# Kernel optimization log

Hardware: AMD Instinct MI355X
Metric: run time of the kernel (lower is better)

Reference implementation:

```python
import jax, jax.numpy as jnp
import numpy as np

D_MODEL = 1024
N_HEADS = 16
DH = (D_MODEL // N_HEADS) // 2  # depth // 2 = 32
B, S = 4, 2048


def setup_inputs() -> dict:
    key = jax.random.key(0)
    ks = jax.random.split(key, 8)
    scale_in = 1.0
    q = jax.random.normal(ks[0], (B, S, D_MODEL), dtype=jnp.float32)
    k = jax.random.normal(ks[1], (B, S, D_MODEL), dtype=jnp.float32)
    v = jax.random.normal(ks[2], (B, S, D_MODEL), dtype=jnp.float32)
    # Per-head projection weights stacked over the head axis (glorot-ish init)
    w_std = (2.0 / (D_MODEL + DH)) ** 0.5
    Wq = jax.random.normal(ks[3], (N_HEADS, D_MODEL, DH), dtype=jnp.float32) * w_std
    Wk = jax.random.normal(ks[4], (N_HEADS, D_MODEL, DH), dtype=jnp.float32) * w_std
    Wv = jax.random.normal(ks[5], (N_HEADS, D_MODEL, DH), dtype=jnp.float32) * w_std
    wo_std = (2.0 / (N_HEADS * DH + D_MODEL)) ** 0.5
    Wo = jax.random.normal(ks[6], (N_HEADS * DH, D_MODEL), dtype=jnp.float32) * wo_std
    return {"q": q, "k": k, "v": v, "Wq": Wq, "Wk": Wk, "Wv": Wv, "Wo": Wo}


def reference(q, k, v, Wq, Wk, Wv, Wo):
    # NOTE: source scales by d_model**-0.5 (not head_dim**-0.5)
    scale = D_MODEL ** (-0.5)
    Q = jnp.einsum("bsd,hde->bhse", q, Wq)   # [B,H,S,DH]
    K = jnp.einsum("btd,hde->bhte", k, Wk)
    V = jnp.einsum("btd,hde->bhte", v, Wv)
    attn = jnp.einsum("bhse,bhte->bhst", Q, K) * scale  # [B,H,S,S]
    attn = jax.nn.softmax(attn, axis=-1)
    x = jnp.einsum("bhst,bhte->bhse", attn, V)  # [B,H,S,DH]
    # concat heads along feature dim (head order = concat order in source)
    x = jnp.transpose(x, (0, 2, 1, 3)).reshape(q.shape[0], q.shape[1], N_HEADS * DH)
    return x @ Wo  # [B,S,D_MODEL]; dropout is identity (training=False)
```

## Files before the change

### kernel.cpp

```cpp
#include <hip/hip_runtime.h>
#include <hip/hip_bf16.h>

typedef __attribute__((ext_vector_type(8))) short short8;
typedef __attribute__((ext_vector_type(4))) float f32x4;
typedef __attribute__((ext_vector_type(4))) float fv4;
typedef __attribute__((ext_vector_type(4))) unsigned int u32x4;

#define MFMA16(a, b, c) __builtin_amdgcn_mfma_f32_16x16x32_bf16((a), (b), (c), 0, 0, 0)

typedef const __attribute__((address_space(1))) unsigned int gu32;
typedef __attribute__((address_space(3))) unsigned int lu32;

__device__ __forceinline__ short f2b(float f) {
  unsigned int x = __builtin_bit_cast(unsigned int, f);
  x += 0x7fffu + ((x >> 16) & 1u);
  return (short)(x >> 16);
}

__device__ __forceinline__ unsigned int cvtpk(float lo, float hi) {
  unsigned int r;
  asm("v_cvt_pk_bf16_f32 %0, %1, %2" : "=v"(r) : "v"(lo), "v"(hi));
  return r;
}

#define hexp2(x) __builtin_amdgcn_exp2f(x)

__global__ void prep_weights(const float* __restrict__ Wq, const float* __restrict__ Wk,
                             const float* __restrict__ Wv, const float* __restrict__ Wo,
                             short* __restrict__ WqT, short* __restrict__ WkT,
                             short* __restrict__ WvT, short* __restrict__ WoT) {
  const float SC2 = 0.045084220027780106f;
  int idx = blockIdx.x * 256 + threadIdx.x;
  if (idx < 3 * 512 * 1024) {
    int wsel = idx >> 19;
    int rem = idx & ((1 << 19) - 1);
    int n = rem >> 10;
    int d = rem & 1023;
    const float* W = (wsel == 0) ? Wq : ((wsel == 1) ? Wk : Wv);
    short* WT = (wsel == 0) ? WqT : ((wsel == 1) ? WkT : WvT);
    float v = W[(n >> 5) * (1024 * 32) + d * 32 + (n & 31)];
    if (wsel == 0) v *= SC2;
    WT[n * 1024 + d] = f2b(v);
  } else {
    int idx2 = idx - 3 * 512 * 1024;
    int n = idx2 >> 9;
    int kk = idx2 & 511;
    WoT[n * 512 + kk] = f2b(Wo[kk * 1024 + n]);
  }
}

__global__ __launch_bounds__(256, 3) void proj_gemm(
    const float* __restrict__ q, const float* __restrict__ k, const float* __restrict__ v,
    const short* __restrict__ WqT, const short* __restrict__ WkT, const short* __restrict__ WvT,
    short* __restrict__ Qb, short* __restrict__ Kb, short* __restrict__ Vtb) {
  __shared__ char smem[49152];
  const int tid = threadIdx.x;
  const int lane = tid & 63;
  const int w = tid >> 6;
  const int l15 = lane & 15, g = lane >> 4;
  const int wm = (w >> 1) * 64, wn = (w & 1) * 64;
  const int id = blockIdx.x;
  const int bm = id & 63;
  const int r = id >> 6;
  const int bn = r & 3;
  const int z = r >> 2;
  const float* A = (z == 0) ? q : ((z == 1) ? k : v);
  const short* BT = (z == 0) ? WqT : ((z == 1) ? WkT : WvT);
  const int bm0 = bm * 128, bn0 = bn * 128;

  const int arow = lane >> 4;
  const int au = lane & 15;
  const int brow = lane >> 3;
  const int bu = lane & 7;

  f32x4 zf = {0.f, 0.f, 0.f, 0.f};
  f32x4 acc[4][4];
#pragma unroll
  for (int a = 0; a < 4; ++a)
#pragma unroll
    for (int bq = 0; bq < 4; ++bq) acc[a][bq] = zf;

  for (int k0 = 0; k0 < 1024; k0 += 64) {
#pragma unroll
    for (int i = 0; i < 8; ++i) {
      int row = 32 * w + 4 * i + arow;
      int u = au ^ (row & 7);
      __builtin_amdgcn_global_load_lds(
          (gu32*)(A + (size_t)(bm0 + row) * 1024 + k0 + 4 * u),
          (lu32*)(smem + w * 8192 + i * 1024), 16, 0, 0);
    }
#pragma unroll
    for (int i = 0; i < 4; ++i) {
      int row = 32 * w + 8 * i + brow;
      int u = bu ^ (row & 7);
      __builtin_amdgcn_global_load_lds(
          (gu32*)(BT + (size_t)(bn0 + row) * 1024 + k0 + 8 * u),
          (lu32*)(smem + 32768 + w * 4096 + i * 1024), 16, 0, 0);
    }
    __syncthreads();

#pragma unroll
    for (int kk = 0; kk < 2; ++kk) {
      short8 af[4], bfr[4];
#pragma unroll
      for (int mf = 0; mf < 4; ++mf) {
        int row = wm + mf * 16 + l15;
        int u0 = 8 * kk + 2 * g;
        fv4 a0 = *(const fv4*)(smem + row * 256 + ((u0 ^ (row & 7)) * 16));
        fv4 a1 = *(const fv4*)(smem + row * 256 + (((u0 + 1) ^ (row & 7)) * 16));
        u32x4 wv;
        wv[0] = cvtpk(a0[0], a0[1]);
        wv[1] = cvtpk(a0[2], a0[3]);
        wv[2] = cvtpk(a1[0], a1[1]);
        wv[3] = cvtpk(a1[2], a1[3]);
        af[mf] = __builtin_bit_cast(short8, wv);
      }
#pragma unroll
      for (int nf = 0; nf < 4; ++nf) {
        int row = wn + nf * 16 + l15;
        int c = 4 * kk + g;
        bfr[nf] = *(const short8*)(smem + 32768 + row * 128 + ((c ^ (row & 7)) * 16));
      }
#pragma unroll
      for (int mf = 0; mf < 4; ++mf)
#pragma unroll
        for (int nf = 0; nf < 4; ++nf)
          acc[mf][nf] = MFMA16(af[mf], bfr[nf], acc[mf][nf]);
    }
    __syncthreads();
  }

#pragma unroll
  for (int mf = 0; mf < 4; ++mf)
#pragma unroll
    for (int nf = 0; nf < 4; ++nf)
#pragma unroll
      for (int i = 0; i < 4; ++i) {
        int row = bm0 + wm + mf * 16 + g * 4 + i;
        int col = bn0 + wn + nf * 16 + l15;
        int bb = row >> 11, ss = row & 2047;
        int hh = col >> 5, ee = col & 31;
        short val = f2b(acc[mf][nf][i]);
        if (z == 2)
          Vtb[((size_t)(bb * 16 + hh) * 32 + ee) * 2048 + ss] = val;
        else if (z == 1)
          Kb[((size_t)(bb * 16 + hh) * 2048 + ss) * 32 + ee] = val;
        else
          Qb[((size_t)(bb * 16 + hh) * 2048 + ss) * 32 + ee] = val;
      }
}

__global__ __launch_bounds__(256, 2) void out_gemm(const short* __restrict__ X,
                                                   const short* __restrict__ WoT,
                                                   float* __restrict__ out) {
  __shared__ char smem[32768];
  const int tid = threadIdx.x;
  const int lane = tid & 63;
  const int w = tid >> 6;
  const int l15 = lane & 15, g = lane >> 4;
  const int wm = (w >> 1) * 64, wn = (w & 1) * 64;
  const int id = blockIdx.x;
  const int bm0 = (id & 63) * 128, bn0 = (id >> 6) * 128;

  const int brow = lane >> 3;
  const int bu = lane & 7;

  f32x4 zf = {0.f, 0.f, 0.f, 0.f};
  f32x4 acc[4][4];
#pragma unroll
  for (int a = 0; a < 4; ++a)
#pragma unroll
    for (int bq = 0; bq < 4; ++bq) acc[a][bq] = zf;

  for (int k0 = 0; k0 < 512; k0 += 64) {
#pragma unroll
    for (int i = 0; i < 4; ++i) {
      int row = 32 * w + 8 * i + brow;
      int u = bu ^ (row & 7);
      __builtin_amdgcn_global_load_lds(
          (gu32*)(X + (size_t)(bm0 + row) * 512 + k0 + 8 * u),
          (lu32*)(smem + w * 4096 + i * 1024), 16, 0, 0);
      __builtin_amdgcn_global_load_lds(
          (gu32*)(WoT + (size_t)(bn0 + row) * 512 + k0 + 8 * u),
          (lu32*)(smem + 16384 + w * 4096 + i * 1024), 16, 0, 0);
    }
    __syncthreads();

#pragma unroll
    for (int kk = 0; kk < 2; ++kk) {
      short8 af[4], bfr[4];
#pragma unroll
      for (int mf = 0; mf < 4; ++mf) {
        int row = wm + mf * 16 + l15;
        int c = 4 * kk + g;
        af[mf] = *(const short8*)(smem + row * 128 + ((c ^ (row & 7)) * 16));
      }
#pragma unroll
      for (int nf = 0; nf < 4; ++nf) {
        int row = wn + nf * 16 + l15;
        int c = 4 * kk + g;
        bfr[nf] = *(const short8*)(smem + 16384 + row * 128 + ((c ^ (row & 7)) * 16));
      }
#pragma unroll
      for (int mf = 0; mf < 4; ++mf)
#pragma unroll
        for (int nf = 0; nf < 4; ++nf)
          acc[mf][nf] = MFMA16(af[mf], bfr[nf], acc[mf][nf]);
    }
    __syncthreads();
  }

#pragma unroll
  for (int mf = 0; mf < 4; ++mf)
#pragma unroll
    for (int nf = 0; nf < 4; ++nf)
#pragma unroll
      for (int i = 0; i < 4; ++i) {
        int row = bm0 + wm + mf * 16 + g * 4 + i;
        int col = bn0 + wn + nf * 16 + l15;
        out[(size_t)row * 1024 + col] = acc[mf][nf][i];
      }
}

__device__ __forceinline__ void qk_half(short8 k0, short8 k1, short8 k2, short8 k3,
                                        short8 qf, const f32x4& zf,
                                        short8& pf0, short8& pf1) {
  f32x4 s0 = MFMA16(k0, qf, zf);
  f32x4 s1 = MFMA16(k1, qf, zf);
  f32x4 s2 = MFMA16(k2, qf, zf);
  f32x4 s3 = MFMA16(k3, qf, zf);
#pragma unroll
  for (int i = 0; i < 4; ++i) {
    s0[i] = hexp2(s0[i]);
    s1[i] = hexp2(s1[i]);
    s2[i] = hexp2(s2[i]);
    s3[i] = hexp2(s3[i]);
  }
  u32x4 w0, w1;
  w0[0] = cvtpk(s0[0], s0[1]);
  w0[1] = cvtpk(s0[2], s0[3]);
  w0[2] = cvtpk(s1[0], s1[1]);
  w0[3] = cvtpk(s1[2], s1[3]);
  w1[0] = cvtpk(s2[0], s2[1]);
  w1[1] = cvtpk(s2[2], s2[3]);
  w1[2] = cvtpk(s3[0], s3[1]);
  w1[3] = cvtpk(s3[2], s3[3]);
  pf0 = __builtin_bit_cast(short8, w0);
  pf1 = __builtin_bit_cast(short8, w1);
}

__global__ __launch_bounds__(256, 4) void attn(const short* __restrict__ Qb,
                                               const short* __restrict__ Kb,
                                               const short* __restrict__ Vtb,
                                               short* __restrict__ X) {
  __shared__ short KV[2][2][2048];
  const int tid = threadIdx.x;
  const int lane = tid & 63;
  const int w = tid >> 6;
  const int l15 = lane & 15, g = lane >> 4;
  const int id = blockIdx.x;
  const int bh = id & 63;
  const int qblk = id >> 6;
  const int bb = bh >> 4, hh = bh & 15;
  const int q0 = qblk * 128 + w * 32;

  const short* Qp = Qb + ((size_t)bh * 2048 + q0) * 32;
  const short* Kp = Kb + (size_t)bh * 2048 * 32;
  const short* Vp = Vtb + (size_t)bh * 32 * 2048;

  short8 qfA = *(const short8*)(Qp + l15 * 32 + g * 8);
  short8 qfB = *(const short8*)(Qp + (16 + l15) * 32 + g * 8);

  const int kbase = 8 * (l15 >> 2) + (l15 & 3);
  const int koff = (w & 1) * 4 + (w >> 1) * 32;
  const int vrow = (w >> 1) * 16;
  const int vcol = (w & 1) * 32;
  const short* Ksrc0 = Kp + (size_t)(kbase + koff) * 32 + g * 8;
  const short* Vsrc0 = Vp + (size_t)(l15 + vrow) * 2048 + vcol + g * 8;

  f32x4 zf = {0.f, 0.f, 0.f, 0.f};
  f32x4 o_loA = zf, o_hiA = zf, o_loB = zf, o_hiB = zf;
  f32x4 accLA = zf, accLB = zf;
  u32x4 ones_u = {0x3F803F80u, 0x3F803F80u, 0x3F803F80u, 0x3F803F80u};
  const short8 ones = __builtin_bit_cast(short8, ones_u);

#define STAGE(b, t0)                                                        \
  {                                                                         \
    __builtin_amdgcn_global_load_lds((gu32*)(Ksrc0 + (size_t)(t0) * 32),    \
                                     (lu32*)&KV[b][0][w * 512], 16, 0, 0);  \
    __builtin_amdgcn_global_load_lds((gu32*)(Vsrc0 + (t0)),                 \
                                     (lu32*)&KV[b][1][w * 512], 16, 0, 0);  \
  }

#define BODY(b)                                                       \
  {                                                                   \
    short8 k0 = *(const short8*)(&KV[b][0][0 * 512 + lane * 8]);      \
    short8 k1 = *(const short8*)(&KV[b][0][1 * 512 + lane * 8]);      \
    short8 k2 = *(const short8*)(&KV[b][0][2 * 512 + lane * 8]);      \
    short8 k3 = *(const short8*)(&KV[b][0][3 * 512 + lane * 8]);      \
    short8 vlo0 = *(const short8*)(&KV[b][1][0 * 512 + lane * 8]);    \
    short8 vlo1 = *(const short8*)(&KV[b][1][1 * 512 + lane * 8]);    \
    short8 vhi0 = *(const short8*)(&KV[b][1][2 * 512 + lane * 8]);    \
    short8 vhi1 = *(const short8*)(&KV[b][1][3 * 512 + lane * 8]);    \
    short8 pfA0, pfA1, pfB0, pfB1;                                    \
    qk_half(k0, k1, k2, k3, qfA, zf, pfA0, pfA1);                     \
    qk_half(k0, k1, k2, k3, qfB, zf, pfB0, pfB1);                     \
    __builtin_amdgcn_s_setprio(1);                                    \
    accLA = MFMA16(pfA0, ones, accLA);                                \
    accLA = MFMA16(pfA1, ones, accLA);                                \
    accLB = MFMA16(pfB0, ones, accLB);                                \
    accLB = MFMA16(pfB1, ones, accLB);                                \
    o_loA = MFMA16(pfA0, vlo0, o_loA);                                \
    o_loA = MFMA16(pfA1, vlo1, o_loA);                                \
    o_hiA = MFMA16(pfA0, vhi0, o_hiA);                                \
    o_hiA = MFMA16(pfA1, vhi1, o_hiA);                                \
    o_loB = MFMA16(pfB0, vlo0, o_loB);                                \
    o_loB = MFMA16(pfB1, vlo1, o_loB);                                \
    o_hiB = MFMA16(pfB0, vhi0, o_hiB);                                \
    o_hiB = MFMA16(pfB1, vhi1, o_hiB);                                \
    __builtin_amdgcn_s_setprio(0);                                    \
  }

  STAGE(0, 0);
  __syncthreads();
  for (int t0 = 0; t0 < 2048; t0 += 128) {
    STAGE(1, t0 + 64);
    BODY(0);
    __syncthreads();
    if (t0 + 128 < 2048) {
      STAGE(0, t0 + 128);
    }
    BODY(1);
    __syncthreads();
  }
#undef STAGE
#undef BODY

#pragma unroll
  for (int i = 0; i < 4; ++i) {
    float invA = 1.0f / accLA[i];
    float invB = 1.0f / accLB[i];
    int ssA = q0 + 4 * g + i;
    size_t baseA = ((size_t)bb * 2048 + ssA) * 512 + hh * 32;
    X[baseA + l15] = f2b(o_loA[i] * invA);
    X[baseA + 16 + l15] = f2b(o_hiA[i] * invA);
    size_t baseB = baseA + (size_t)16 * 512;
    X[baseB + l15] = f2b(o_loB[i] * invB);
    X[baseB + 16 + l15] = f2b(o_hiB[i] * invB);
  }
}

extern "C" void kernel_launch(void* const* d_in, const int* in_sizes, int n_in,
                              void* d_out, int out_size, void* d_ws, size_t ws_size,
                              hipStream_t stream) {
  const float* q = (const float*)d_in[0];
  const float* k = (const float*)d_in[1];
  const float* v = (const float*)d_in[2];
  const float* Wq = (const float*)d_in[3];
  const float* Wk = (const float*)d_in[4];
  const float* Wv = (const float*)d_in[5];
  const float* Wo = (const float*)d_in[6];

  char* ws = (char*)d_ws;
  const size_t MB = 1u << 20;
  short* WqT = (short*)(ws + 0 * MB);
  short* WkT = (short*)(ws + 1 * MB);
  short* WvT = (short*)(ws + 2 * MB);
  short* WoT = (short*)(ws + 3 * MB);
  short* Qb  = (short*)(ws + 4 * MB);
  short* Kb  = (short*)(ws + 12 * MB);
  short* Vtb = (short*)(ws + 20 * MB);
  short* Xb  = (short*)(ws + 28 * MB);

  prep_weights<<<8192, 256, 0, stream>>>(Wq, Wk, Wv, Wo, WqT, WkT, WvT, WoT);
  proj_gemm<<<768, 256, 0, stream>>>(q, k, v, WqT, WkT, WvT, Qb, Kb, Vtb);
  attn<<<1024, 256, 0, stream>>>(Qb, Kb, Vtb, Xb);
  out_gemm<<<512, 256, 0, stream>>>(Xb, WoT, (float*)d_out);
}
```

Measured before the change: 123.1 us.

## Double-buffer projection and output GEMMs; convert fp32 A to bf16 before LDS staging

After: 122.6 us. No clear change (-0.4%).

```diff
diff --git a/kernel.cpp b/kernel.cpp
--- a/kernel.cpp
+++ b/kernel.cpp
@@ -7,6 +7,7 @@
 typedef __attribute__((ext_vector_type(4))) unsigned int u32x4;
 
 #define MFMA16(a, b, c) __builtin_amdgcn_mfma_f32_16x16x32_bf16((a), (b), (c), 0, 0, 0)
+#define SBAR() __builtin_amdgcn_sched_barrier(0)
 
 typedef const __attribute__((address_space(1))) unsigned int gu32;
 typedef __attribute__((address_space(3))) unsigned int lu32;
@@ -53,7 +54,7 @@
     const float* __restrict__ q, const float* __restrict__ k, const float* __restrict__ v,
     const short* __restrict__ WqT, const short* __restrict__ WkT, const short* __restrict__ WvT,
     short* __restrict__ Qb, short* __restrict__ Kb, short* __restrict__ Vtb) {
-  __shared__ char smem[49152];
+  __shared__ char smem[32768];
   const int tid = threadIdx.x;
   const int lane = tid & 63;
   const int w = tid >> 6;
@@ -68,10 +69,17 @@
   const short* BT = (z == 0) ? WqT : ((z == 1) ? WkT : WvT);
   const int bm0 = bm * 128, bn0 = bn * 128;
 
-  const int arow = lane >> 4;
-  const int au = lane & 15;
-  const int brow = lane >> 3;
-  const int bu = lane & 7;
+  const int arow = w * 32 + (lane >> 1);
+  const int ahalf = lane & 1;
+  const int aswz = (arow >> 1) & 3;
+  const float* Ag = A + (size_t)(bm0 + arow) * 1024 + ahalf * 16;
+  const int aw_off0 = arow * 64 + (((2 * ahalf) ^ aswz) * 16);
+  const int aw_off1 = arow * 64 + (((2 * ahalf + 1) ^ aswz) * 16);
+
+  const int brow0 = w * 32 + (lane >> 2);
+  const int brow1 = brow0 + 16;
+  const short* Bg0 = BT + (size_t)(bn0 + brow0) * 1024 + 8 * ((lane & 3) ^ ((brow0 >> 1) & 3));
+  const short* Bg1 = BT + (size_t)(bn0 + brow1) * 1024 + 8 * ((lane & 3) ^ ((brow1 >> 1) & 3));
 
   f32x4 zf = {0.f, 0.f, 0.f, 0.f};
   f32x4 acc[4][4];
@@ -80,55 +88,78 @@
 #pragma unroll
     for (int bq = 0; bq < 4; ++bq) acc[a][bq] = zf;
 
-  for (int k0 = 0; k0 < 1024; k0 += 64) {
-#pragma unroll
-    for (int i = 0; i < 8; ++i) {
-      int row = 32 * w + 4 * i + arow;
-      int u = au ^ (row & 7);
-      __builtin_amdgcn_global_load_lds(
-          (gu32*)(A + (size_t)(bm0 + row) * 1024 + k0 + 4 * u),
-          (lu32*)(smem + w * 8192 + i * 1024), 16, 0, 0);
+  fv4 fa0, fa1, fa2, fa3;
+#define GLOADA(k0)                          \
+  fa0 = *(const fv4*)(Ag + (k0));           \
+  fa1 = *(const fv4*)(Ag + (k0) + 4);       \
+  fa2 = *(const fv4*)(Ag + (k0) + 8);       \
+  fa3 = *(const fv4*)(Ag + (k0) + 12);
+
+#define WRITEA(aoff)                                                  \
+  {                                                                   \
+    u32x4 wv0, wv1;                                                   \
+    wv0[0] = cvtpk(fa0[0], fa0[1]);                                   \
+    wv0[1] = cvtpk(fa0[2], fa0[3]);                                   \
+    wv0[2] = cvtpk(fa1[0], fa1[1]);                                   \
+    wv0[3] = cvtpk(fa1[2], fa1[3]);                                   \
+    wv1[0] = cvtpk(fa2[0], fa2[1]);                                   \
+    wv1[1] = cvtpk(fa2[2], fa2[3]);                                   \
+    wv1[2] = cvtpk(fa3[0], fa3[1]);                                   \
+    wv1[3] = cvtpk(fa3[2], fa3[3]);                                   \
+    *(short8*)(smem + (aoff) + aw_off0) = __builtin_bit_cast(short8, wv0); \
+    *(short8*)(smem + (aoff) + aw_off1) = __builtin_bit_cast(short8, wv1); \
+  }
+
+#define STAGEB(boff, k0)                                                      \
+  {                                                                           \
+    __builtin_amdgcn_global_load_lds((gu32*)(Bg0 + (k0)),                     \
+                                     (lu32*)(smem + (boff) + w * 2048), 16, 0, 0); \
+    __builtin_amdgcn_global_load_lds((gu32*)(Bg1 + (k0)),                     \
+                                     (lu32*)(smem + (boff) + w * 2048 + 1024), 16, 0, 0); \
+  }
+
+#define COMPUTE(aoff, boff)                                                    \
+  {                                                                            \
+    short8 af[4], bfr[4];                                                      \
+    _Pragma("unroll") for (int mf = 0; mf < 4; ++mf) {                         \
+      int ar = wm + mf * 16 + l15;                                             \
+      af[mf] = *(const short8*)(smem + (aoff) + ar * 64 +                      \
+                                ((g ^ ((ar >> 1) & 3)) * 16));                 \
+    }                                                                          \
+    _Pragma("unroll") for (int nf = 0; nf < 4; ++nf) {                         \
+      int br = wn + nf * 16 + l15;                                             \
+      bfr[nf] = *(const short8*)(smem + (boff) + br * 64 +                     \
+                                 ((g ^ ((br >> 1) & 3)) * 16));                \
+    }                                                                          \
+    _Pragma("unroll") for (int mf = 0; mf < 4; ++mf)                           \
+        _Pragma("unroll") for (int nf = 0; nf < 4; ++nf)                       \
+            acc[mf][nf] = MFMA16(af[mf], bfr[nf], acc[mf][nf]);                \
+  }
+
+  GLOADA(0);
+  STAGEB(16384, 0);
+  WRITEA(0);
+  __syncthreads();
+
+  for (int k0 = 0; k0 < 1024; k0 += 32) {
+    const int cur = (k0 >> 5) & 1;
+    const int nxt = cur ^ 1;
+    const int acur = cur * 8192, anxt = nxt * 8192;
+    const int bcur = 16384 + cur * 8192, bnxt = 16384 + nxt * 8192;
+    if (k0 + 32 < 1024) {
+      GLOADA(k0 + 32);
+      STAGEB(bnxt, k0 + 32);
     }
-#pragma unroll
-    for (int i = 0; i < 4; ++i) {
-      int row = 32 * w + 8 * i + brow;
-      int u = bu ^ (row & 7);
-      __builtin_amdgcn_global_load_lds(
-          (gu32*)(BT + (size_t)(bn0 + row) * 1024 + k0 + 8 * u),
-          (lu32*)(smem + 32768 + w * 4096 + i * 1024), 16, 0, 0);
-    }
+    SBAR();
+    COMPUTE(acur, bcur);
+    SBAR();
+    if (k0 + 32 < 1024) WRITEA(anxt);
     __syncthreads();
-
-#pragma unroll
-    for (int kk = 0; kk < 2; ++kk) {
-      short8 af[4], bfr[4];
-#pragma unroll
-      for (int mf = 0; mf < 4; ++mf) {
-        int row = wm + mf * 16 + l15;
-        int u0 = 8 * kk + 2 * g;
-        fv4 a0 = *(const fv4*)(smem + row * 256 + ((u0 ^ (row & 7)) * 16));
-        fv4 a1 = *(const fv4*)(smem + row * 256 + (((u0 + 1) ^ (row & 7)) * 16));
-        u32x4 wv;
-        wv[0] = cvtpk(a0[0], a0[1]);
-        wv[1] = cvtpk(a0[2], a0[3]);
-        wv[2] = cvtpk(a1[0], a1[1]);
-        wv[3] = cvtpk(a1[2], a1[3]);
-        af[mf] = __builtin_bit_cast(short8, wv);
-      }
-#pragma unroll
-      for (int nf = 0; nf < 4; ++nf) {
-        int row = wn + nf * 16 + l15;
-        int c = 4 * kk + g;
-        bfr[nf] = *(const short8*)(smem + 32768 + row * 128 + ((c ^ (row & 7)) * 16));
-      }
-#pragma unroll
-      for (int mf = 0; mf < 4; ++mf)
-#pragma unroll
-        for (int nf = 0; nf < 4; ++nf)
-          acc[mf][nf] = MFMA16(af[mf], bfr[nf], acc[mf][nf]);
-    }
-    __syncthreads();
-  }
+  }
+#undef GLOADA
+#undef WRITEA
+#undef STAGEB
+#undef COMPUTE
 
 #pragma unroll
   for (int mf = 0; mf < 4; ++mf)
@@ -162,8 +193,13 @@
   const int id = blockIdx.x;
   const int bm0 = (id & 63) * 128, bn0 = (id >> 6) * 128;
 
-  const int brow = lane >> 3;
-  const int bu = lane & 7;
+  const int row0 = w * 32 + (lane >> 2);
+  const int row1 = row0 + 16;
+  const int sl = lane & 3;
+  const short* Ag0 = X + (size_t)(bm0 + row0) * 512 + 8 * (sl ^ ((row0 >> 1) & 3));
+  const short* Ag1 = X + (size_t)(bm0 + row1) * 512 + 8 * (sl ^ ((row1 >> 1) & 3));
+  const short* Bg0 = WoT + (size_t)(bn0 + row0) * 512 + 8 * (sl ^ ((row0 >> 1) & 3));
+  const short* Bg1 = WoT + (size_t)(bn0 + row1) * 512 + 8 * (sl ^ ((row1 >> 1) & 3));
 
   f32x4 zf = {0.f, 0.f, 0.f, 0.f};
   f32x4 acc[4][4];
@@ -172,43 +208,51 @@
 #pragma unroll
     for (int bq = 0; bq < 4; ++bq) acc[a][bq] = zf;
 
-  for (int k0 = 0; k0 < 512; k0 += 64) {
-#pragma unroll
-    for (int i = 0; i < 4; ++i) {
-      int row = 32 * w + 8 * i + brow;
-      int u = bu ^ (row & 7);
-      __builtin_amdgcn_global_load_lds(
-          (gu32*)(X + (size_t)(bm0 + row) * 512 + k0 + 8 * u),
-          (lu32*)(smem + w * 4096 + i * 1024), 16, 0, 0);
-      __builtin_amdgcn_global_load_lds(
-          (gu32*)(WoT + (size_t)(bn0 + row) * 512 + k0 + 8 * u),
-          (lu32*)(smem + 16384 + w * 4096 + i * 1024), 16, 0, 0);
+#define STAGE(aoff, boff, k0)                                                     \
+  {                                                                               \
+    __builtin_amdgcn_global_load_lds((gu32*)(Ag0 + (k0)),                         \
+                                     (lu32*)(smem + (aoff) + w * 2048), 16, 0, 0); \
+    __builtin_amdgcn_global_load_lds((gu32*)(Ag1 + (k0)),                         \
+                                     (lu32*)(smem + (aoff) + w * 2048 + 1024), 16, 0, 0); \
+    __builtin_amdgcn_global_load_lds((gu32*)(Bg0 + (k0)),                         \
+                                     (lu32*)(smem + (boff) + w * 2048), 16, 0, 0); \
+    __builtin_amdgcn_global_load_lds((gu32*)(Bg1 + (k0)),                         \
+                                     (lu32*)(smem + (boff) + w * 2048 + 1024), 16, 0, 0); \
+  }
+
+#define COMPUTE(aoff, boff)                                                    \
+  {                                                                            \
+    short8 af[4], bfr[4];                                                      \
+    _Pragma("unroll") for (int mf = 0; mf < 4; ++mf) {                         \
+      int ar = wm + mf * 16 + l15;                                             \
+      af[mf] = *(const short8*)(smem + (aoff) + ar * 64 +                      \
+                                ((g ^ ((ar >> 1) & 3)) * 16));                 \
+    }                                                                          \
+    _Pragma("unroll") for (int nf = 0; nf < 4; ++nf) {                         \
+      int br = wn + nf * 16 + l15;                                             \
+      bfr[nf] = *(const short8*)(smem + (boff) + br * 64 +                     \
+                                 ((g ^ ((br >> 1) & 3)) * 16));                \
+    }                                                                          \
+    _Pragma("unroll") for (int mf = 0; mf < 4; ++mf)                           \
+        _Pragma("unroll") for (int nf = 0; nf < 4; ++nf)                       \
+            acc[mf][nf] = MFMA16(af[mf], bfr[nf], acc[mf][nf]);                \
+  }
+
+  STAGE(0, 16384, 0);
+  __syncthreads();
+  for (int k0 = 0; k0 < 512; k0 += 32) {
+    const int cur = (k0 >> 5) & 1;
+    const int nxt = cur ^ 1;
+    if (k0 + 32 < 512) {
+      STAGE(nxt * 8192, 16384 + nxt * 8192, k0 + 32);
     }
+    SBAR();
+    COMPUTE(cur * 8192, 16384 + cur * 8192);
+    SBAR();
     __syncthreads();
-
-#pragma unroll
-    for (int kk = 0; kk < 2; ++kk) {
-      short8 af[4], bfr[4];
-#pragma unroll
-      for (int mf = 0; mf < 4; ++mf) {
-        int row = wm + mf * 16 + l15;
-        int c = 4 * kk + g;
-        af[mf] = *(const short8*)(smem + row * 128 + ((c ^ (row & 7)) * 16));
-      }
-#pragma unroll
-      for (int nf = 0; nf < 4; ++nf) {
-        int row = wn + nf * 16 + l15;
-        int c = 4 * kk + g;
-        bfr[nf] = *(const short8*)(smem + 16384 + row * 128 + ((c ^ (row & 7)) * 16));
-      }
-#pragma unroll
-      for (int mf = 0; mf < 4; ++mf)
-#pragma unroll
-        for (int nf = 0; nf < 4; ++nf)
-          acc[mf][nf] = MFMA16(af[mf], bfr[nf], acc[mf][nf]);
-    }
-    __syncthreads();
-  }
+  }
+#undef STAGE
+#undef COMPUTE
 
 #pragma unroll
   for (int mf = 0; mf < 4; ++mf)
```
